# Performance work log

Hardware: AMD Instinct MI355X
Metric: run time of the kernel (lower is better)

The kernel has to match this reference:

```python
import jax, jax.numpy as jnp
import numpy as np

B, S, H, F, E, TOPK = 2, 2048, 1024, 4096, 8, 2


def setup_inputs() -> dict:
    key = jax.random.key(0)
    k0, k1, k2, k3, k4 = jax.random.split(key, 5)
    scale = 0.02
    return {
        "hidden_states": jax.random.normal(k0, (B, S, H), dtype=jnp.float32),
        "gate_w": jax.random.normal(k1, (E, H), dtype=jnp.float32) * scale,
        "w1": jax.random.normal(k2, (E, F, H), dtype=jnp.float32) * scale,
        "w2": jax.random.normal(k3, (E, H, F), dtype=jnp.float32) * scale,
        "w3": jax.random.normal(k4, (E, F, H), dtype=jnp.float32) * scale,
        "top_k": TOPK,
    }


def reference(hidden_states, gate_w, w1, w2, w3, top_k):
    b, s, h = hidden_states.shape
    num_experts = gate_w.shape[0]
    x = hidden_states.reshape(-1, h)                      # [T,H]
    router_logits = x @ gate_w.T                          # [T,E]
    routing = jax.nn.softmax(router_logits.astype(jnp.float32), axis=-1)
    top_w, top_e = jax.lax.top_k(routing, top_k)          # [T,K]
    top_w = top_w / top_w.sum(axis=-1, keepdims=True)     # renormalize over top-k
    top_w = top_w.astype(x.dtype)
    # combine weights [T,E]: zero for unselected experts (faithful to masked dispatch)
    cw = (jax.nn.one_hot(top_e, num_experts, dtype=x.dtype) * top_w[..., None]).sum(axis=1)
    out = jnp.zeros_like(x)
    for e in range(num_experts):  # fixed, small expert count
        inter = jax.nn.silu(x @ w1[e].T) * (x @ w3[e].T)  # [T,F]
        out = out + cw[:, e:e + 1] * (inter @ w2[e].T)
    return out.reshape(b, s, h), router_logits
```

## Files before the change

kernel.cpp:

```cpp
#include <hip/hip_runtime.h>
#include <stdint.h>

#define T 4096
#define HDIM 1024
#define FDIM 4096
#define NE 8
#define MAXROWS 10240

typedef __bf16 bf16x8 __attribute__((ext_vector_type(8)));
typedef float f32x4 __attribute__((ext_vector_type(4)));

__device__ __forceinline__ unsigned short f2bf(float f) {
    unsigned u = __builtin_bit_cast(unsigned, f);
    u += 0x7FFFu + ((u >> 16) & 1u);
    return (unsigned short)(u >> 16);
}

__device__ __forceinline__ void cp16(const void* g, const void* lds) {
    __builtin_amdgcn_global_load_lds(
        (const __attribute__((address_space(1))) unsigned int*)g,
        (__attribute__((address_space(3))) unsigned int*)(unsigned int)(unsigned long long)lds,
        16, 0, 0);
}

__global__ void conv_x_k(const float* __restrict__ x, unsigned short* __restrict__ xb) {
    size_t i = ((size_t)blockIdx.x * 256 + threadIdx.x) * 8;
    float4 a = *(const float4*)(x + i);
    float4 b = *(const float4*)(x + i + 4);
    uint4 v;
    v.x = (unsigned)f2bf(a.x) | ((unsigned)f2bf(a.y) << 16);
    v.y = (unsigned)f2bf(a.z) | ((unsigned)f2bf(a.w) << 16);
    v.z = (unsigned)f2bf(b.x) | ((unsigned)f2bf(b.y) << 16);
    v.w = (unsigned)f2bf(b.z) | ((unsigned)f2bf(b.w) << 16);
    *(uint4*)(xb + i) = v;
}

__global__ void conv_all_k(const float* __restrict__ w1, const float* __restrict__ w3,
                           const float* __restrict__ w2,
                           unsigned short* __restrict__ wb1, unsigned short* __restrict__ wb3,
                           unsigned short* __restrict__ wb2) {
    int z = blockIdx.y;
    const float* s = (z == 0) ? w1 : (z == 1) ? w3 : w2;
    unsigned short* d = (z == 0) ? wb1 : (z == 1) ? wb3 : wb2;
    size_t i = ((size_t)blockIdx.x * 256 + threadIdx.x) * 8;
    float4 a = *(const float4*)(s + i);
    float4 b = *(const float4*)(s + i + 4);
    uint4 v;
    v.x = (unsigned)f2bf(a.x) | ((unsigned)f2bf(a.y) << 16);
    v.y = (unsigned)f2bf(a.z) | ((unsigned)f2bf(a.w) << 16);
    v.z = (unsigned)f2bf(b.x) | ((unsigned)f2bf(b.y) << 16);
    v.w = (unsigned)f2bf(b.z) | ((unsigned)f2bf(b.w) << 16);
    *(uint4*)(d + i) = v;
}

__global__ void conv_w13_k(const float* __restrict__ src, unsigned short* __restrict__ dst,
                           int f0, int Fc) {
    int e = blockIdx.y;
    size_t rem = ((size_t)blockIdx.x * 256 + threadIdx.x) * 8;
    const float* s = src + ((size_t)e * FDIM + f0) * HDIM + rem;
    unsigned short* d = dst + (size_t)e * Fc * HDIM + rem;
    float4 a = *(const float4*)(s);
    float4 b = *(const float4*)(s + 4);
    uint4 v;
    v.x = (unsigned)f2bf(a.x) | ((unsigned)f2bf(a.y) << 16);
    v.y = (unsigned)f2bf(a.z) | ((unsigned)f2bf(a.w) << 16);
    v.z = (unsigned)f2bf(b.x) | ((unsigned)f2bf(b.y) << 16);
    v.w = (unsigned)f2bf(b.z) | ((unsigned)f2bf(b.w) << 16);
    *(uint4*)(d) = v;
}

__global__ void conv_w2_k(const float* __restrict__ src, unsigned short* __restrict__ dst,
                          int f0, int Fc, int fcShift) {
    int e = blockIdx.y;
    size_t idx = ((size_t)blockIdx.x * 256 + threadIdx.x) * 8;
    int h = (int)(idx >> fcShift);
    int c = (int)(idx & (size_t)(Fc - 1));
    const float* s = src + ((size_t)e * HDIM + h) * FDIM + f0 + c;
    unsigned short* d = dst + (size_t)e * HDIM * Fc + idx;
    float4 a = *(const float4*)(s);
    float4 b = *(const float4*)(s + 4);
    uint4 v;
    v.x = (unsigned)f2bf(a.x) | ((unsigned)f2bf(a.y) << 16);
    v.y = (unsigned)f2bf(a.z) | ((unsigned)f2bf(a.w) << 16);
    v.z = (unsigned)f2bf(b.x) | ((unsigned)f2bf(b.y) << 16);
    v.w = (unsigned)f2bf(b.z) | ((unsigned)f2bf(b.w) << 16);
    *(uint4*)(d) = v;
}

__global__ __launch_bounds__(1024) void router_k(
    const float* __restrict__ x, const float* __restrict__ gw,
    float* __restrict__ logits_out, int* __restrict__ cnt,
    int* __restrict__ list, float* __restrict__ wlist) {
    __shared__ int   ltok[128];
    __shared__ int   lexp[128];
    __shared__ float lww[128];
    __shared__ int   lpos[128];
    __shared__ int   bcnt[NE];
    __shared__ int   bbase[NE];

    int tid = threadIdx.x, wave = tid >> 6, lane = tid & 63;
    if (tid < NE) bcnt[tid] = 0;

#pragma unroll 1
    for (int j = 0; j < 4; ++j) {
        int t = blockIdx.x * 64 + wave * 4 + j;
        float acc[NE];
#pragma unroll
        for (int e = 0; e < NE; ++e) acc[e] = 0.f;
        for (int i = 0; i < HDIM / 64; ++i) {
            int h = i * 64 + lane;
            float xv = x[(size_t)t * HDIM + h];
#pragma unroll
            for (int e = 0; e < NE; ++e) acc[e] += xv * gw[e * HDIM + h];
        }
#pragma unroll
        for (int e = 0; e < NE; ++e)
#pragma unroll
            for (int off = 32; off; off >>= 1) acc[e] += __shfl_xor(acc[e], off);
        if (lane == 0) {
#pragma unroll
            for (int e = 0; e < NE; ++e) logits_out[(size_t)t * NE + e] = acc[e];
            int e1 = 0;
#pragma unroll
            for (int e = 1; e < NE; ++e) if (acc[e] > acc[e1]) e1 = e;
            int e2 = (e1 == 0) ? 1 : 0;
#pragma unroll
            for (int e = 0; e < NE; ++e) { if (e == e1) continue; if (acc[e] > acc[e2]) e2 = e; }
            float wa = 1.f / (1.f + expf(acc[e2] - acc[e1]));
            float wb = 1.f - wa;
            int s = (wave * 4 + j) * 2;
            ltok[s] = t;     lexp[s] = e1;     lww[s] = wa;
            ltok[s + 1] = t; lexp[s + 1] = e2; lww[s + 1] = wb;
        }
    }
    __syncthreads();
    if (tid < 128) lpos[tid] = atomicAdd(&bcnt[lexp[tid]], 1);
    __syncthreads();
    if (tid < NE) bbase[tid] = atomicAdd(&cnt[tid], bcnt[tid]);
    __syncthreads();
    if (tid < 128) {
        int e = lexp[tid];
        int p = bbase[e] + lpos[tid];
        list[e * T + p] = ltok[tid];
        wlist[e * T + p] = lww[tid];
    }
}

__global__ void offsets_k(const int* __restrict__ cnt, int* __restrict__ poff) {
    if (threadIdx.x == 0) {
        int o = 0; poff[0] = 0;
        for (int e = 0; e < NE; ++e) { o += ((cnt[e] + 255) >> 8) << 8; poff[e + 1] = o; }
    }
}

__global__ void compact_k(const int* __restrict__ cnt, const int* __restrict__ poff,
                          const int* __restrict__ list, const float* __restrict__ wlist,
                          int* __restrict__ tok_row, float* __restrict__ w_row) {
    int gid = blockIdx.x * 256 + threadIdx.x;
    int e = gid >> 12, i = gid & (T - 1);
    int pc = poff[e + 1] - poff[e];
    if (i < pc) {
        int row = poff[e] + i;
        if (i < cnt[e]) { tok_row[row] = list[e * T + i]; w_row[row] = wlist[e * T + i]; }
        else           { tok_row[row] = T;               w_row[row] = 0.f; }
    }
}

__global__ __launch_bounds__(512, 2) void gemm1_k(
    const unsigned short* __restrict__ xb, const unsigned short* __restrict__ wb1,
    const unsigned short* __restrict__ wb3, const int* __restrict__ tok_row,
    const int* __restrict__ poff, unsigned short* __restrict__ inter, int Fc) {

    __shared__ __align__(16) unsigned short lds[2 * 32768];
    __shared__ int toks[256];
    __shared__ int e_sh;

    int row0 = blockIdx.y * 256;
    if (row0 >= poff[NE]) return;
    int tid = threadIdx.x;
    if (tid == 0) { int e = 0; while (row0 >= poff[e + 1]) ++e; e_sh = e; }
    if (tid < 256) toks[tid] = tok_row[row0 + tid];
    __syncthreads();
    int e = e_sh;
    int fr0 = blockIdx.x * 128;
    const unsigned short* w1p = wb1 + ((size_t)e * Fc + fr0) * HDIM;
    const unsigned short* w3p = wb3 + ((size_t)e * Fc + fr0) * HDIM;

    int wv = tid >> 6, lane = tid & 63;
    int quad = lane >> 4, l16 = lane & 15;
    int wm = (wv >> 1) * 64;
    int wn = (wv & 1) * 64;

    int sr = lane >> 3;
    int sc = (lane & 7) ^ sr;
    unsigned a_off[4];
#pragma unroll
    for (int jj = 0; jj < 4; ++jj)
        a_off[jj] = (unsigned)toks[(wv * 4 + jj) * 8 + sr] * HDIM + sc * 8;
    const unsigned short* b1b = w1p + (size_t)(wv * 16 + sr) * HDIM + sc * 8;
    const unsigned short* b3b = w3p + (size_t)(wv * 16 + sr) * HDIM + sc * 8;

    char* ldsc = (char*)lds;
    unsigned dstA  = (unsigned)(wv * 4) * 1024u;
    unsigned dstB1 = 32768u + (unsigned)(wv * 2) * 1024u;
    unsigned dstB3 = 49152u + (unsigned)(wv * 2) * 1024u;

    f32x4 acc1[4][4], acc3[4][4];
#pragma unroll
    for (int a = 0; a < 4; ++a)
#pragma unroll
        for (int b = 0; b < 4; ++b) {
            acc1[a][b] = f32x4{0.f, 0.f, 0.f, 0.f};
            acc3[a][b] = f32x4{0.f, 0.f, 0.f, 0.f};
        }

#pragma unroll
    for (int jj = 0; jj < 4; ++jj)
        cp16(xb + a_off[jj], ldsc + dstA + jj * 1024);
#pragma unroll
    for (int jj = 0; jj < 2; ++jj) {
        cp16(b1b + (size_t)jj * 8 * HDIM, ldsc + dstB1 + jj * 1024);
        cp16(b3b + (size_t)jj * 8 * HDIM, ldsc + dstB3 + jj * 1024);
    }
    __syncthreads();

#pragma unroll 1
    for (int k = 0; k < 16; ++k) {
        const unsigned short* sb = lds + (k & 1) * 32768;

        if (k < 15) {
            char* db = ldsc + ((k + 1) & 1) * 65536;
            int ko = (k + 1) * 64;
#pragma unroll
            for (int jj = 0; jj < 4; ++jj)
                cp16(xb + a_off[jj] + ko, db + dstA + jj * 1024);
#pragma unroll
            for (int jj = 0; jj < 2; ++jj) {
                cp16(b1b + (size_t)jj * 8 * HDIM + ko, db + dstB1 + jj * 1024);
                cp16(b3b + (size_t)jj * 8 * HDIM + ko, db + dstB3 + jj * 1024);
            }
        }

#pragma unroll
        for (int ks = 0; ks < 2; ++ks) {
            int cb0 = ks * 4 + quad;
            bf16x8 af[4], b1f[4], b3f[4];
#pragma unroll
            for (int mi = 0; mi < 4; ++mi) {
                int m = wm + mi * 16 + l16;
                af[mi] = *(const bf16x8*)(sb + m * 64 + ((cb0 ^ (m & 7)) * 8));
            }
#pragma unroll
            for (int ni = 0; ni < 4; ++ni) {
                int n = wn + ni * 16 + l16;
                int sw = (cb0 ^ (n & 7)) * 8;
                b1f[ni] = *(const bf16x8*)(sb + 16384 + n * 64 + sw);
                b3f[ni] = *(const bf16x8*)(sb + 24576 + n * 64 + sw);
            }
            __builtin_amdgcn_s_setprio(1);
#pragma unroll
            for (int ni = 0; ni < 4; ++ni)
#pragma unroll
                for (int mi = 0; mi < 4; ++mi) {
                    acc1[mi][ni] = __builtin_amdgcn_mfma_f32_16x16x32_bf16(af[mi], b1f[ni], acc1[mi][ni], 0, 0, 0);
                    acc3[mi][ni] = __builtin_amdgcn_mfma_f32_16x16x32_bf16(af[mi], b3f[ni], acc3[mi][ni], 0, 0, 0);
                }
            __builtin_amdgcn_s_setprio(0);
        }
        __syncthreads();
    }

#pragma unroll
    for (int mi = 0; mi < 4; ++mi)
#pragma unroll
        for (int ni = 0; ni < 4; ++ni)
#pragma unroll
            for (int r = 0; r < 4; ++r) {
                int m = wm + mi * 16 + quad * 4 + r;
                int n = wn + ni * 16 + l16;
                float v1 = acc1[mi][ni][r], v3 = acc3[mi][ni][r];
                float hval = (v1 / (1.f + __expf(-v1))) * v3;
                inter[(size_t)(row0 + m) * Fc + fr0 + n] = f2bf(hval);
            }
}

__global__ __launch_bounds__(256, 2) void gemm2_k(
    const unsigned short* __restrict__ inter, const unsigned short* __restrict__ wb2,
    const int* __restrict__ tok_row, const float* __restrict__ w_row,
    const int* __restrict__ poff, float* __restrict__ out, int Fc) {

    __shared__ __align__(16) unsigned short lds[2 * 16384];
    __shared__ int e_sh;

    int bx = blockIdx.x, by = blockIdx.y;
    int Xn = by & 7;
    int Ys = (by >> 3) * 8 + bx;

    int row0 = Ys * 128;
    if (row0 >= poff[NE]) return;
    int tid = threadIdx.x;
    if (tid == 0) { int e = 0; while (row0 >= poff[e + 1]) ++e; e_sh = e; }
    __syncthreads();
    int e = e_sh;
    int n0 = Xn * 128;

    int wv = tid >> 6, lane = tid & 63;
    int quad = lane >> 4, l16 = lane & 15;
    int wm = (wv >> 1) * 64, wn = (wv & 1) * 64;

    int sr = lane >> 3;
    int sc = (lane & 7) ^ sr;
    const unsigned short* a_b = inter + (size_t)(row0 + wv * 32 + sr) * Fc + sc * 8;
    const unsigned short* b_b = wb2 + ((size_t)e * HDIM + n0 + wv * 32 + sr) * Fc + sc * 8;

    char* ldsc = (char*)lds;

    f32x4 acc[4][4];
#pragma unroll
    for (int a = 0; a < 4; ++a)
#pragma unroll
        for (int b = 0; b < 4; ++b) acc[a][b] = f32x4{0.f, 0.f, 0.f, 0.f};

#pragma unroll
    for (int jj = 0; jj < 4; ++jj) {
        int j = wv * 4 + jj;
        cp16(a_b + (size_t)jj * 8 * Fc, ldsc + j * 1024);
        cp16(b_b + (size_t)jj * 8 * Fc, ldsc + 16384 + j * 1024);
    }
    __syncthreads();

#pragma unroll 1
    for (int k = 0; k < 64; ++k) {
        const unsigned short* sb = lds + (k & 1) * 16384;

        if (k < 63) {
            char* db = ldsc + ((k + 1) & 1) * 32768;
            int ko = (k + 1) * 64;
#pragma unroll
            for (int jj = 0; jj < 4; ++jj) {
                int j = wv * 4 + jj;
                cp16(a_b + (size_t)jj * 8 * Fc + ko, db + j * 1024);
                cp16(b_b + (size_t)jj * 8 * Fc + ko, db + 16384 + j * 1024);
            }
        }

#pragma unroll
        for (int ks = 0; ks < 2; ++ks) {
            int cb0 = ks * 4 + quad;
            bf16x8 af[4];
#pragma unroll
            for (int mi = 0; mi < 4; ++mi) {
                int m = wm + mi * 16 + l16;
                af[mi] = *(const bf16x8*)(sb + m * 64 + ((cb0 ^ (m & 7)) * 8));
            }
#pragma unroll
            for (int ni = 0; ni < 4; ++ni) {
                int n = wn + ni * 16 + l16;
                bf16x8 bf = *(const bf16x8*)(sb + 8192 + n * 64 + ((cb0 ^ (n & 7)) * 8));
#pragma unroll
                for (int mi = 0; mi < 4; ++mi)
                    acc[mi][ni] = __builtin_amdgcn_mfma_f32_16x16x32_bf16(af[mi], bf, acc[mi][ni], 0, 0, 0);
            }
        }
        __syncthreads();
    }

#pragma unroll
    for (int mi = 0; mi < 4; ++mi)
#pragma unroll
        for (int r = 0; r < 4; ++r) {
            int m = wm + mi * 16 + quad * 4 + r;
            int grow = row0 + m;
            float wr = w_row[grow];
            if (wr != 0.f) {
                int t = tok_row[grow];
                float* op = out + (size_t)t * HDIM + n0;
#pragma unroll
                for (int ni = 0; ni < 4; ++ni)
                    atomicAdd(op + wn + ni * 16 + l16, wr * acc[mi][ni][r]);
            }
        }
}

extern "C" void kernel_launch(void* const* d_in, const int* in_sizes, int n_in,
                              void* d_out, int out_size, void* d_ws, size_t ws_size,
                              hipStream_t stream) {
    const float* x  = (const float*)d_in[0];
    const float* gw = (const float*)d_in[1];
    const float* w1 = (const float*)d_in[2];
    const float* w2 = (const float*)d_in[3];
    const float* w3 = (const float*)d_in[4];
    float* out = (float*)d_out;
    float* logits = out + (size_t)T * HDIM;

    char* ws = (char*)d_ws;
    size_t off = 0;
    auto alloc = [&](size_t b) {
        off = (off + 255) & ~(size_t)255;
        void* p = ws + off;
        off += b;
        return p;
    };
    int* cnt        = (int*)alloc(NE * 4);
    int* poff       = (int*)alloc((NE + 1) * 4);
    int* list       = (int*)alloc((size_t)NE * T * 4);
    float* wlist    = (float*)alloc((size_t)NE * T * 4);
    int* tok_row    = (int*)alloc(MAXROWS * 4);
    float* w_row    = (float*)alloc(MAXROWS * 4);
    unsigned short* xb = (unsigned short*)alloc((size_t)(T + 1) * HDIM * 2);
    size_t fixed_off = off;

    int Fc = 4096, fcShift = 12;
    for (;;) {
        size_t need = fixed_off + 3 * ((size_t)NE * Fc * HDIM * 2) + (size_t)MAXROWS * Fc * 2 + 1024;
        if (need <= ws_size || Fc == 512) break;
        Fc >>= 1; fcShift -= 1;
    }
    unsigned short* wb1 = (unsigned short*)alloc((size_t)NE * Fc * HDIM * 2);
    unsigned short* wb3 = (unsigned short*)alloc((size_t)NE * Fc * HDIM * 2);
    unsigned short* wb2 = (unsigned short*)alloc((size_t)NE * HDIM * Fc * 2);
    unsigned short* inter = (unsigned short*)alloc((size_t)MAXROWS * Fc * 2);

    hipMemsetAsync(cnt, 0, NE * 4, stream);
    hipMemsetAsync(out, 0, (size_t)T * HDIM * 4, stream);
    hipMemsetAsync(xb + (size_t)T * HDIM, 0, HDIM * 2, stream);
    conv_x_k<<<(T * HDIM / 8) / 256, 256, 0, stream>>>(x, xb);
    router_k<<<T / 64, 1024, 0, stream>>>(x, gw, logits, cnt, list, wlist);
    offsets_k<<<1, 64, 0, stream>>>(cnt, poff);
    compact_k<<<NE * T / 256, 256, 0, stream>>>(cnt, poff, list, wlist, tok_row, w_row);

    int nMT1 = MAXROWS / 256;
    int nMT2 = MAXROWS / 128;
    if (Fc == FDIM) {
        conv_all_k<<<dim3((size_t)NE * FDIM * HDIM / 8 / 256, 3), 256, 0, stream>>>(
            w1, w3, w2, wb1, wb3, wb2);
        gemm1_k<<<dim3(FDIM / 128, nMT1), 512, 0, stream>>>(xb, wb1, wb3, tok_row, poff, inter, FDIM);
        gemm2_k<<<dim3(HDIM / 128, nMT2), 256, 0, stream>>>(inter, wb2, tok_row, w_row, poff, out, FDIM);
    } else {
        for (int f0 = 0; f0 < FDIM; f0 += Fc) {
            conv_w13_k<<<dim3(Fc / 2, NE), 256, 0, stream>>>(w1, wb1, f0, Fc);
            conv_w13_k<<<dim3(Fc / 2, NE), 256, 0, stream>>>(w3, wb3, f0, Fc);
            conv_w2_k<<<dim3(HDIM * Fc / 2048, NE), 256, 0, stream>>>(w2, wb2, f0, Fc, fcShift);
            gemm1_k<<<dim3(Fc / 128, nMT1), 512, 0, stream>>>(xb, wb1, wb3, tok_row, poff, inter, Fc);
            gemm2_k<<<dim3(HDIM / 128, nMT2), 256, 0, stream>>>(inter, wb2, tok_row, w_row, poff, out, Fc);
        }
    }
}
```

Baseline: 755.5 us.

## Fuse fp32-to-bf16 weight conversion into expert GEMM tile loads

```diff
diff --git a/kernel.cpp b/kernel.cpp
--- a/kernel.cpp
+++ b/kernel.cpp
@@ -14,6 +14,13 @@
     unsigned u = __builtin_bit_cast(unsigned, f);
     u += 0x7FFFu + ((u >> 16) & 1u);
     return (unsigned short)(u >> 16);
+}
+
+__device__ __forceinline__ bf16x8 cvt8(float4 a, float4 b) {
+    bf16x8 r;
+    r[0] = (__bf16)a.x; r[1] = (__bf16)a.y; r[2] = (__bf16)a.z; r[3] = (__bf16)a.w;
+    r[4] = (__bf16)b.x; r[5] = (__bf16)b.y; r[6] = (__bf16)b.z; r[7] = (__bf16)b.w;
+    return r;
 }
 
 __device__ __forceinline__ void cp16(const void* g, const void* lds) {
@@ -35,58 +42,6 @@
     *(uint4*)(xb + i) = v;
 }
 
-__global__ void conv_all_k(const float* __restrict__ w1, const float* __restrict__ w3,
-                           const float* __restrict__ w2,
-                           unsigned short* __restrict__ wb1, unsigned short* __restrict__ wb3,
-                           unsigned short* __restrict__ wb2) {
-    int z = blockIdx.y;
-    const float* s = (z == 0) ? w1 : (z == 1) ? w3 : w2;
-    unsigned short* d = (z == 0) ? wb1 : (z == 1) ? wb3 : wb2;
-    size_t i = ((size_t)blockIdx.x * 256 + threadIdx.x) * 8;
-    float4 a = *(const float4*)(s + i);
-    float4 b = *(const float4*)(s + i + 4);
-    uint4 v;
-    v.x = (unsigned)f2bf(a.x) | ((unsigned)f2bf(a.y) << 16);
-    v.y = (unsigned)f2bf(a.z) | ((unsigned)f2bf(a.w) << 16);
-    v.z = (unsigned)f2bf(b.x) | ((unsigned)f2bf(b.y) << 16);
-    v.w = (unsigned)f2bf(b.z) | ((unsigned)f2bf(b.w) << 16);
-    *(uint4*)(d + i) = v;
-}
-
-__global__ void conv_w13_k(const float* __restrict__ src, unsigned short* __restrict__ dst,
-                           int f0, int Fc) {
-    int e = blockIdx.y;
-    size_t rem = ((size_t)blockIdx.x * 256 + threadIdx.x) * 8;
-    const float* s = src + ((size_t)e * FDIM + f0) * HDIM + rem;
-    unsigned short* d = dst + (size_t)e * Fc * HDIM + rem;
-    float4 a = *(const float4*)(s);
-    float4 b = *(const float4*)(s + 4);
-    uint4 v;
-    v.x = (unsigned)f2bf(a.x) | ((unsigned)f2bf(a.y) << 16);
-    v.y = (unsigned)f2bf(a.z) | ((unsigned)f2bf(a.w) << 16);
-    v.z = (unsigned)f2bf(b.x) | ((unsigned)f2bf(b.y) << 16);
-    v.w = (unsigned)f2bf(b.z) | ((unsigned)f2bf(b.w) << 16);
-    *(uint4*)(d) = v;
-}
-
-__global__ void conv_w2_k(const float* __restrict__ src, unsigned short* __restrict__ dst,
-                          int f0, int Fc, int fcShift) {
-    int e = blockIdx.y;
-    size_t idx = ((size_t)blockIdx.x * 256 + threadIdx.x) * 8;
-    int h = (int)(idx >> fcShift);
-    int c = (int)(idx & (size_t)(Fc - 1));
-    const float* s = src + ((size_t)e * HDIM + h) * FDIM + f0 + c;
-    unsigned short* d = dst + (size_t)e * HDIM * Fc + idx;
-    float4 a = *(const float4*)(s);
-    float4 b = *(const float4*)(s + 4);
-    uint4 v;
-    v.x = (unsigned)f2bf(a.x) | ((unsigned)f2bf(a.y) << 16);
-    v.y = (unsigned)f2bf(a.z) | ((unsigned)f2bf(a.w) << 16);
-    v.z = (unsigned)f2bf(b.x) | ((unsigned)f2bf(b.y) << 16);
-    v.w = (unsigned)f2bf(b.z) | ((unsigned)f2bf(b.w) << 16);
-    *(uint4*)(d) = v;
-}
-
 __global__ __launch_bounds__(1024) void router_k(
     const float* __restrict__ x, const float* __restrict__ gw,
     float* __restrict__ logits_out, int* __restrict__ cnt,
@@ -167,8 +122,8 @@
 }
 
 __global__ __launch_bounds__(512, 2) void gemm1_k(
-    const unsigned short* __restrict__ xb, const unsigned short* __restrict__ wb1,
-    const unsigned short* __restrict__ wb3, const int* __restrict__ tok_row,
+    const unsigned short* __restrict__ xb, const float* __restrict__ w1,
+    const float* __restrict__ w3, const int* __restrict__ tok_row,
     const int* __restrict__ poff, unsigned short* __restrict__ inter, int Fc) {
 
     __shared__ __align__(16) unsigned short lds[2 * 32768];
@@ -183,8 +138,8 @@
     __syncthreads();
     int e = e_sh;
     int fr0 = blockIdx.x * 128;
-    const unsigned short* w1p = wb1 + ((size_t)e * Fc + fr0) * HDIM;
-    const unsigned short* w3p = wb3 + ((size_t)e * Fc + fr0) * HDIM;
+    const float* w1p = w1 + ((size_t)e * FDIM + fr0) * HDIM;
+    const float* w3p = w3 + ((size_t)e * FDIM + fr0) * HDIM;
 
     int wv = tid >> 6, lane = tid & 63;
     int quad = lane >> 4, l16 = lane & 15;
@@ -197,13 +152,13 @@
 #pragma unroll
     for (int jj = 0; jj < 4; ++jj)
         a_off[jj] = (unsigned)toks[(wv * 4 + jj) * 8 + sr] * HDIM + sc * 8;
-    const unsigned short* b1b = w1p + (size_t)(wv * 16 + sr) * HDIM + sc * 8;
-    const unsigned short* b3b = w3p + (size_t)(wv * 16 + sr) * HDIM + sc * 8;
+    const float* b1b = w1p + (size_t)(wv * 16 + sr) * HDIM + sc * 8;
+    const float* b3b = w3p + (size_t)(wv * 16 + sr) * HDIM + sc * 8;
 
     char* ldsc = (char*)lds;
-    unsigned dstA  = (unsigned)(wv * 4) * 1024u;
-    unsigned dstB1 = 32768u + (unsigned)(wv * 2) * 1024u;
-    unsigned dstB3 = 49152u + (unsigned)(wv * 2) * 1024u;
+    unsigned dstA = (unsigned)(wv * 4) * 1024u;
+    unsigned wB1  = 32768u + (unsigned)(wv * 2) * 1024u + (unsigned)lane * 16u;
+    unsigned wB3  = wB1 + 16384u;
 
     f32x4 acc1[4][4], acc3[4][4];
 #pragma unroll
@@ -217,10 +172,19 @@
 #pragma unroll
     for (int jj = 0; jj < 4; ++jj)
         cp16(xb + a_off[jj], ldsc + dstA + jj * 1024);
-#pragma unroll
-    for (int jj = 0; jj < 2; ++jj) {
-        cp16(b1b + (size_t)jj * 8 * HDIM, ldsc + dstB1 + jj * 1024);
-        cp16(b3b + (size_t)jj * 8 * HDIM, ldsc + dstB3 + jj * 1024);
+    {
+        float4 p0 = *(const float4*)(b1b);
+        float4 p1 = *(const float4*)(b1b + 4);
+        float4 p2 = *(const float4*)(b1b + (size_t)8 * HDIM);
+        float4 p3 = *(const float4*)(b1b + (size_t)8 * HDIM + 4);
+        float4 p4 = *(const float4*)(b3b);
+        float4 p5 = *(const float4*)(b3b + 4);
+        float4 p6 = *(const float4*)(b3b + (size_t)8 * HDIM);
+        float4 p7 = *(const float4*)(b3b + (size_t)8 * HDIM + 4);
+        *(bf16x8*)(ldsc + wB1)        = cvt8(p0, p1);
+        *(bf16x8*)(ldsc + wB1 + 1024) = cvt8(p2, p3);
+        *(bf16x8*)(ldsc + wB3)        = cvt8(p4, p5);
+        *(bf16x8*)(ldsc + wB3 + 1024) = cvt8(p6, p7);
     }
     __syncthreads();
 
@@ -228,17 +192,21 @@
     for (int k = 0; k < 16; ++k) {
         const unsigned short* sb = lds + (k & 1) * 32768;
 
+        float4 q0, q1, q2, q3, q4, q5, q6, q7;
         if (k < 15) {
             char* db = ldsc + ((k + 1) & 1) * 65536;
             int ko = (k + 1) * 64;
 #pragma unroll
             for (int jj = 0; jj < 4; ++jj)
                 cp16(xb + a_off[jj] + ko, db + dstA + jj * 1024);
-#pragma unroll
-            for (int jj = 0; jj < 2; ++jj) {
-                cp16(b1b + (size_t)jj * 8 * HDIM + ko, db + dstB1 + jj * 1024);
-                cp16(b3b + (size_t)jj * 8 * HDIM + ko, db + dstB3 + jj * 1024);
-            }
+            q0 = *(const float4*)(b1b + ko);
+            q1 = *(const float4*)(b1b + ko + 4);
+            q2 = *(const float4*)(b1b + (size_t)8 * HDIM + ko);
+            q3 = *(const float4*)(b1b + (size_t)8 * HDIM + ko + 4);
+            q4 = *(const float4*)(b3b + ko);
+            q5 = *(const float4*)(b3b + ko + 4);
+            q6 = *(const float4*)(b3b + (size_t)8 * HDIM + ko);
+            q7 = *(const float4*)(b3b + (size_t)8 * HDIM + ko + 4);
         }
 
 #pragma unroll
@@ -266,6 +234,14 @@
                     acc3[mi][ni] = __builtin_amdgcn_mfma_f32_16x16x32_bf16(af[mi], b3f[ni], acc3[mi][ni], 0, 0, 0);
                 }
             __builtin_amdgcn_s_setprio(0);
+        }
+
+        if (k < 15) {
+            char* db = ldsc + ((k + 1) & 1) * 65536;
+            *(bf16x8*)(db + wB1)        = cvt8(q0, q1);
+            *(bf16x8*)(db + wB1 + 1024) = cvt8(q2, q3);
+            *(bf16x8*)(db + wB3)        = cvt8(q4, q5);
+            *(bf16x8*)(db + wB3 + 1024) = cvt8(q6, q7);
         }
         __syncthreads();
     }
@@ -285,7 +261,7 @@
 }
 
 __global__ __launch_bounds__(256, 2) void gemm2_k(
-    const unsigned short* __restrict__ inter, const unsigned short* __restrict__ wb2,
+    const unsigned short* __restrict__ inter, const float* __restrict__ w2,
     const int* __restrict__ tok_row, const float* __restrict__ w_row,
     const int* __restrict__ poff, float* __restrict__ out, int Fc) {
 
@@ -311,9 +287,10 @@
     int sr = lane >> 3;
     int sc = (lane & 7) ^ sr;
     const unsigned short* a_b = inter + (size_t)(row0 + wv * 32 + sr) * Fc + sc * 8;
-    const unsigned short* b_b = wb2 + ((size_t)e * HDIM + n0 + wv * 32 + sr) * Fc + sc * 8;
+    const float* b_b = w2 + ((size_t)e * HDIM + n0 + wv * 32 + sr) * FDIM + sc * 8;
 
     char* ldsc = (char*)lds;
+    unsigned wB = 16384u + (unsigned)(wv * 4) * 1024u + (unsigned)lane * 16u;
 
     f32x4 acc[4][4];
 #pragma unroll
@@ -322,26 +299,36 @@
         for (int b = 0; b < 4; ++b) acc[a][b] = f32x4{0.f, 0.f, 0.f, 0.f};
 
 #pragma unroll
+    for (int jj = 0; jj < 4; ++jj)
+        cp16(a_b + (size_t)jj * 8 * Fc, ldsc + (wv * 4 + jj) * 1024);
+#pragma unroll
     for (int jj = 0; jj < 4; ++jj) {
-        int j = wv * 4 + jj;
-        cp16(a_b + (size_t)jj * 8 * Fc, ldsc + j * 1024);
-        cp16(b_b + (size_t)jj * 8 * Fc, ldsc + 16384 + j * 1024);
-    }
-    __syncthreads();
-
+        float4 p0 = *(const float4*)(b_b + (size_t)jj * 8 * FDIM);
+        float4 p1 = *(const float4*)(b_b + (size_t)jj * 8 * FDIM + 4);
+        *(bf16x8*)(ldsc + wB + jj * 1024) = cvt8(p0, p1);
+    }
+    __syncthreads();
+
+    int nk = Fc >> 6;
 #pragma unroll 1
-    for (int k = 0; k < 64; ++k) {
+    for (int k = 0; k < nk; ++k) {
         const unsigned short* sb = lds + (k & 1) * 16384;
 
-        if (k < 63) {
+        float4 q0, q1, q2, q3, q4, q5, q6, q7;
+        if (k < nk - 1) {
             char* db = ldsc + ((k + 1) & 1) * 32768;
             int ko = (k + 1) * 64;
 #pragma unroll
-            for (int jj = 0; jj < 4; ++jj) {
-                int j = wv * 4 + jj;
-                cp16(a_b + (size_t)jj * 8 * Fc + ko, db + j * 1024);
-                cp16(b_b + (size_t)jj * 8 * Fc + ko, db + 16384 + j * 1024);
-            }
+            for (int jj = 0; jj < 4; ++jj)
+                cp16(a_b + (size_t)jj * 8 * Fc + ko, db + (wv * 4 + jj) * 1024);
+            q0 = *(const float4*)(b_b + ko);
+            q1 = *(const float4*)(b_b + ko + 4);
+            q2 = *(const float4*)(b_b + (size_t)8 * FDIM + ko);
+            q3 = *(const float4*)(b_b + (size_t)8 * FDIM + ko + 4);
+            q4 = *(const float4*)(b_b + (size_t)16 * FDIM + ko);
+            q5 = *(const float4*)(b_b + (size_t)16 * FDIM + ko + 4);
+            q6 = *(const float4*)(b_b + (size_t)24 * FDIM + ko);
+            q7 = *(const float4*)(b_b + (size_t)24 * FDIM + ko + 4);
         }
 
 #pragma unroll
@@ -361,6 +348,14 @@
                 for (int mi = 0; mi < 4; ++mi)
                     acc[mi][ni] = __builtin_amdgcn_mfma_f32_16x16x32_bf16(af[mi], bf, acc[mi][ni], 0, 0, 0);
             }
+        }
+
+        if (k < nk - 1) {
+            char* db = ldsc + ((k + 1) & 1) * 32768;
+            *(bf16x8*)(db + wB)        = cvt8(q0, q1);
+            *(bf16x8*)(db + wB + 1024) = cvt8(q2, q3);
+            *(bf16x8*)(db + wB + 2048) = cvt8(q4, q5);
+            *(bf16x8*)(db + wB + 3072) = cvt8(q6, q7);
         }
         __syncthreads();
     }
@@ -410,15 +405,12 @@
     unsigned short* xb = (unsigned short*)alloc((size_t)(T + 1) * HDIM * 2);
     size_t fixed_off = off;
 
-    int Fc = 4096, fcShift = 12;
+    int Fc = 4096;
     for (;;) {
-        size_t need = fixed_off + 3 * ((size_t)NE * Fc * HDIM * 2) + (size_t)MAXROWS * Fc * 2 + 1024;
+        size_t need = fixed_off + (size_t)MAXROWS * Fc * 2 + 1024;
         if (need <= ws_size || Fc == 512) break;
-        Fc >>= 1; fcShift -= 1;
-    }
-    unsigned short* wb1 = (unsigned short*)alloc((size_t)NE * Fc * HDIM * 2);
-    unsigned short* wb3 = (unsigned short*)alloc((size_t)NE * Fc * HDIM * 2);
-    unsigned short* wb2 = (unsigned short*)alloc((size_t)NE * HDIM * Fc * 2);
+        Fc >>= 1;
+    }
     unsigned short* inter = (unsigned short*)alloc((size_t)MAXROWS * Fc * 2);
 
     hipMemsetAsync(cnt, 0, NE * 4, stream);
@@ -431,18 +423,10 @@
 
     int nMT1 = MAXROWS / 256;
     int nMT2 = MAXROWS / 128;
-    if (Fc == FDIM) {
-        conv_all_k<<<dim3((size_t)NE * FDIM * HDIM / 8 / 256, 3), 256, 0, stream>>>(
-            w1, w3, w2, wb1, wb3, wb2);
-        gemm1_k<<<dim3(FDIM / 128, nMT1), 512, 0, stream>>>(xb, wb1, wb3, tok_row, poff, inter, FDIM);
-        gemm2_k<<<dim3(HDIM / 128, nMT2), 256, 0, stream>>>(inter, wb2, tok_row, w_row, poff, out, FDIM);
-    } else {
-        for (int f0 = 0; f0 < FDIM; f0 += Fc) {
-            conv_w13_k<<<dim3(Fc / 2, NE), 256, 0, stream>>>(w1, wb1, f0, Fc);
-            conv_w13_k<<<dim3(Fc / 2, NE), 256, 0, stream>>>(w3, wb3, f0, Fc);
-            conv_w2_k<<<dim3(HDIM * Fc / 2048, NE), 256, 0, stream>>>(w2, wb2, f0, Fc, fcShift);
-            gemm1_k<<<dim3(Fc / 128, nMT1), 512, 0, stream>>>(xb, wb1, wb3, tok_row, poff, inter, Fc);
-            gemm2_k<<<dim3(HDIM / 128, nMT2), 256, 0, stream>>>(inter, wb2, tok_row, w_row, poff, out, Fc);
-        }
-    }
-}
+    for (int f0 = 0; f0 < FDIM; f0 += Fc) {
+        gemm1_k<<<dim3(Fc / 128, nMT1), 512, 0, stream>>>(
+            xb, w1 + (size_t)f0 * HDIM, w3 + (size_t)f0 * HDIM, tok_row, poff, inter, Fc);
+        gemm2_k<<<dim3(HDIM / 128, nMT2), 256, 0, stream>>>(
+            inter, w2 + f0, tok_row, w_row, poff, out, Fc);
+    }
+}
```

After: 856.7 us. 1.13x slower.
